# Kernel tuning notes

Measured on AMD Instinct MI355X. Metric: run time of the kernel, lower is better.

## Reference

```python
import jax, jax.numpy as jnp
import numpy as np

MS0 = 4            # base sector size (ms[0])
MS1 = 4            # top sector size (r=[1] -> ms[-1]=ms0)
Q = 2              # q_length (Ising spin states)
C = 512            # c_length
LAYERS = 2
B = 256
L = 16
FS = MS0 * MS0 - 1  # neighborhood size, excludes target pixel


def setup_inputs():
    key = jax.random.key(0)
    ks = jax.random.split(key, 8)
    v = jax.random.randint(ks[0], (B, L, L), 0, Q, dtype=jnp.int32)
    u = v.astype(jnp.float32)
    emb = jax.random.normal(ks[1], (FS, Q, C), dtype=jnp.float32)  # fs embedding tables

    def lin_w(k, out_d, in_d):
        b = 1.0 / np.sqrt(in_d)
        return jax.random.uniform(k, (out_d, in_d), minval=-b, maxval=b, dtype=jnp.float32)

    def lin_b(k, out_d, in_d):
        b = 1.0 / np.sqrt(in_d)
        return jax.random.uniform(k, (out_d,), minval=-b, maxval=b, dtype=jnp.float32)

    k2a, k2b = jax.random.split(ks[2])
    k3a, k3b = jax.random.split(ks[3])
    mlp_w1 = lin_w(k2a, C, C)
    mlp_b1 = lin_b(k2b, C, C)
    mlp_w2 = lin_w(k3a, Q, C)
    mlp_b2 = lin_b(k3b, Q, C)

    def lstm_p(k, in_d):
        k1, k2, k3, k4 = jax.random.split(k, 4)
        b = 1.0 / np.sqrt(C)
        wi = jax.random.uniform(k1, (4 * C, in_d), minval=-b, maxval=b, dtype=jnp.float32)
        wh = jax.random.uniform(k2, (4 * C, C), minval=-b, maxval=b, dtype=jnp.float32)
        bi = jax.random.uniform(k3, (4 * C,), minval=-b, maxval=b, dtype=jnp.float32)
        bh = jax.random.uniform(k4, (4 * C,), minval=-b, maxval=b, dtype=jnp.float32)
        return wi, wh, bi, bh

    w_ih0, w_hh0, b_ih0, b_hh0 = lstm_p(ks[4], MS1 * MS1)
    w_ih1, w_hh1, b_ih1, b_hh1 = lstm_p(ks[5], C)
    return dict(u=u, v=v, emb=emb,
                mlp_w1=mlp_w1, mlp_b1=mlp_b1, mlp_w2=mlp_w2, mlp_b2=mlp_b2,
                w_ih0=w_ih0, w_hh0=w_hh0, b_ih0=b_ih0, b_hh0=b_hh0,
                w_ih1=w_ih1, w_hh1=w_hh1, b_ih1=b_ih1, b_hh1=b_hh1)


def _forward(u, v, emb, mlp_w1, mlp_b1, mlp_w2, mlp_b2,
             w_ih0, w_hh0, b_ih0, b_hh0, w_ih1, w_hh1, b_ih1, b_hh1):
    n_sec = L // MS0
    margin = MS0 - 1
    lstm_params = ((w_ih0, w_hh0, b_ih0, b_hh0), (w_ih1, w_hh1, b_ih1, b_hh1))

    def lstm_step(x, state):
        # single-timestep multi-layer LSTM (eval mode, no dropout)
        h, c = state  # [LAYERS, B, C] each
        hs, cs = [], []
        inp = x
        for l, (wi, wh, bi, bh) in enumerate(lstm_params):
            g = inp @ wi.T + bi + h[l] @ wh.T + bh
            gi, gf, gg, go = jnp.split(g, 4, axis=-1)  # torch gate order i,f,g,o
            cn = jax.nn.sigmoid(gf) * c[l] + jax.nn.sigmoid(gi) * jnp.tanh(gg)
            hn = jax.nn.sigmoid(go) * jnp.tanh(cn)
            hs.append(hn)
            cs.append(cn)
            inp = hn
        return (jnp.stack(hs), jnp.stack(cs))

    zeros_state = lambda: (jnp.zeros((LAYERS, B, C), jnp.float32),
                           jnp.zeros((LAYERS, B, C), jnp.float32))
    memi = [zeros_state() for _ in range(n_sec)]
    memj = [zeros_state() for _ in range(n_sec)]
    sector = [0, 0]
    softout = jnp.zeros((B, L, L, Q), jnp.float32)
    nbr = jnp.arange(FS)[None, :]  # [1, FS] embedding-table indices
    key = jax.random.key(1234)

    for i in range(n_sec - 1):
        for j in range(n_sec - 1):
            si, sj = i * MS0, j * MS0
            ns0, ns1 = MS1 * (si // MS1), MS1 * (sj // MS1)
            if ns1 != sector[1]:
                sector = [ns0, ns1]
                for s in range(n_sec):
                    uv = u[:, s * MS1:(s + 1) * MS1, sector[1]:sector[1] + MS1].reshape(B, MS1 * MS1)
                    memj[s] = lstm_step(uv, memj[s])
            if ns0 != sector[0]:
                sector[0] = ns0
                uv = u[:, sector[0] - MS1:sector[0], sector[1]:sector[1] + MS1].reshape(B, MS1 * MS1)
                memi[sector[0] // MS1] = lstm_step(uv, memi[sector[0] // MS1])
            h0 = memj[i][0][0] + memi[j][0][0]  # layer-0 hidden sum, [B, C]
            for ii in range(MS0):
                for jj in range(MS0):
                    a, b = si + ii + 1, sj + jj + 1
                    pr, pc = a + margin, b + margin  # target pixel (bottom-right of patch)
                    patch = v[:, a:a + MS0, b:b + MS0].reshape(B, MS0 * MS0)[:, :FS]  # mask drops (margin,margin)
                    xemb = emb[nbr, patch, :].sum(axis=1)  # [B, C]
                    z = jax.nn.relu((xemb + h0) @ mlp_w1.T + mlp_b1)
                    logits = jax.nn.log_softmax(z @ mlp_w2.T + mlp_b2, axis=-1)  # [B, Q]
                    softout = softout.at[:, pr, pc].set(logits)
                    key, sub = jax.random.split(key)
                    samp = jax.random.categorical(sub, logits, axis=-1)  # [B]
                    v = v.at[:, pr, pc].set(samp.astype(v.dtype))
                    u = u.at[:, pr, pc].set(samp.astype(u.dtype))
    return softout, u, v


def reference(u, v, emb, mlp_w1, mlp_b1, mlp_w2, mlp_b2,
              w_ih0, w_hh0, b_ih0, b_hh0, w_ih1, w_hh1, b_ih1, b_hh1):
    return _forward(u, v, emb, mlp_w1, mlp_b1, mlp_w2, mlp_b2,
                    w_ih0, w_hh0, b_ih0, b_hh0, w_ih1, w_hh1, b_ih1, b_hh1)
```

## Files before the change

kernel.cpp:

```cpp
#include <hip/hip_runtime.h>
#include <cstdint>
#include <cstddef>

constexpr int NB = 256;
constexpr int NC = 512;
constexpr int NL = 16;
constexpr int NFS = 15;

#define PARTITIONABLE 1

struct TFOut { uint32_t a, b; };

__host__ __device__ constexpr uint32_t rotl32(uint32_t x, int d) {
  return (x << d) | (x >> (32 - d));
}

__host__ __device__ constexpr TFOut tf2x32(uint32_t k0, uint32_t k1,
                                           uint32_t x0, uint32_t x1) {
  uint32_t k2 = k0 ^ k1 ^ 0x1BD11BDAu;
  x0 += k0; x1 += k1;
  const int R0[4] = {13, 15, 26, 6};
  const int R1[4] = {17, 29, 16, 24};
  for (int i = 0; i < 4; i++) { x0 += x1; x1 = rotl32(x1, R0[i]); x1 ^= x0; }
  x0 += k1; x1 += k2 + 1u;
  for (int i = 0; i < 4; i++) { x0 += x1; x1 = rotl32(x1, R1[i]); x1 ^= x0; }
  x0 += k2; x1 += k0 + 2u;
  for (int i = 0; i < 4; i++) { x0 += x1; x1 = rotl32(x1, R0[i]); x1 ^= x0; }
  x0 += k0; x1 += k1 + 3u;
  for (int i = 0; i < 4; i++) { x0 += x1; x1 = rotl32(x1, R1[i]); x1 ^= x0; }
  x0 += k1; x1 += k2 + 4u;
  for (int i = 0; i < 4; i++) { x0 += x1; x1 = rotl32(x1, R0[i]); x1 ^= x0; }
  x0 += k2; x1 += k0 + 5u;
  return TFOut{x0, x1};
}

struct SubKeys { uint32_t v[288]; };

constexpr SubKeys make_subkeys() {
  SubKeys s{};
  uint32_t k0 = 0u, k1 = 1234u;
  for (int t = 0; t < 144; t++) {
#if PARTITIONABLE
    TFOut nk = tf2x32(k0, k1, 0u, 0u);
    TFOut sk = tf2x32(k0, k1, 0u, 1u);
    s.v[2 * t] = sk.a; s.v[2 * t + 1] = sk.b;
    k0 = nk.a; k1 = nk.b;
#else
    TFOut p0 = tf2x32(k0, k1, 0u, 2u);
    TFOut p1 = tf2x32(k0, k1, 1u, 3u);
    s.v[2 * t] = p0.b; s.v[2 * t + 1] = p1.b;
    k0 = p0.a; k1 = p1.a;
#endif
  }
  return s;
}

__constant__ SubKeys SUBKEYS = make_subkeys();

__device__ __forceinline__ float gumbel_from_bits(uint32_t bits) {
  uint32_t ub = (bits >> 9) | 0x3f800000u;
  float f = __uint_as_float(ub) - 1.0f;
  float u = (f == 0.0f) ? 1.17549435e-38f : f;
  float inner = logf(u);
  float outer = logf(-inner);
  return -outer;
}

typedef __attribute__((ext_vector_type(8))) short bf16x8;
typedef __attribute__((ext_vector_type(4))) float f32x4;

__device__ __forceinline__ void gl2lds16(const unsigned short* g,
                                         unsigned short* l) {
  __builtin_amdgcn_global_load_lds(
      (const __attribute__((address_space(1))) unsigned int*)g,
      (__attribute__((address_space(3))) unsigned int*)l, 16, 0, 0);
}

__device__ __forceinline__ uint32_t bf_rne(float x) {
  uint32_t u = __float_as_uint(x);
  return (u + 0x7fffu + ((u >> 16) & 1u)) >> 16;
}

__device__ __forceinline__ uint32_t bfpack2(float a, float b) {
  return (bf_rne(a) & 0xffffu) | (bf_rne(b) << 16);
}

__global__ __launch_bounds__(256) void setup_kernel(
    const float* __restrict__ u_in, const int* __restrict__ v_in,
    float* __restrict__ h0buf, float* __restrict__ cbuf,
    float* __restrict__ u_cur, int* __restrict__ v_cur,
    float* __restrict__ out_soft, float* __restrict__ out_u,
    float* __restrict__ out_v, unsigned int* __restrict__ az) {
  int idx = blockIdx.x * 256 + threadIdx.x;
  h0buf[idx] = 0.0f;
  if (idx < 3 * NB * NC) cbuf[idx] = 0.0f;
  if (idx < 393216) az[idx] = 0u;
  if (idx < NB * NL * NL) {
    float uv = u_in[idx];
    int vv = v_in[idx];
    u_cur[idx] = uv;
    v_cur[idx] = vv;
    out_u[idx] = uv;
    out_v[idx] = (float)vv;
  }
  if (idx < NB * NL * NL * 2) out_soft[idx] = 0.0f;
}

__global__ __launch_bounds__(256) void split_w_kernel(
    const float* __restrict__ whh, const float* __restrict__ wih,
    unsigned short* __restrict__ Bhi, unsigned short* __restrict__ Blo,
    unsigned short* __restrict__ Buh, unsigned short* __restrict__ Bul) {
  int idx = blockIdx.x * 256 + threadIdx.x;
  float x = whh[idx];
  uint32_t hb = bf_rne(x);
  float lo = x - __uint_as_float(hb << 16);
  Bhi[idx] = (unsigned short)hb;
  Blo[idx] = (unsigned short)bf_rne(lo);
  if (idx < 2048 * 16) {
    float y = wih[idx];
    uint32_t hb2 = bf_rne(y);
    float lo2 = y - __uint_as_float(hb2 << 16);
    Buh[idx] = (unsigned short)hb2;
    Bul[idx] = (unsigned short)bf_rne(lo2);
  }
}

__global__ __launch_bounds__(256) void wd_kernel(
    const float* __restrict__ emb, const float* __restrict__ w1,
    const float* __restrict__ b1, float* __restrict__ WD,
    float* __restrict__ A0v) {
  __shared__ double dvec[NC];
  int n = blockIdx.x, tid = threadIdx.x;
  for (int k = tid; k < NC; k += 256) {
    if (n < NFS) {
      dvec[k] = (double)emb[(n * 2 + 1) * NC + k] - (double)emb[(n * 2) * NC + k];
    } else {
      double s = 0.0;
      for (int nn = 0; nn < NFS; nn++) s += (double)emb[(nn * 2) * NC + k];
      dvec[k] = s;
    }
  }
  __syncthreads();
  for (int c = tid; c < NC; c += 256) {
    double acc = 0.0;
    const float* wrow = w1 + (size_t)c * NC;
    for (int k = 0; k < NC; k++) acc += dvec[k] * (double)wrow[k];
    if (n < NFS) WD[n * NC + c] = (float)acc;
    else         A0v[c] = (float)(acc + (double)b1[c]);
  }
}

__global__ __launch_bounds__(256) void lstm_mfma_kernel(
    const unsigned short* __restrict__ Ahi, const unsigned short* __restrict__ Alo,
    const unsigned short* __restrict__ Bhi, const unsigned short* __restrict__ Blo,
    const unsigned short* __restrict__ Buh, const unsigned short* __restrict__ Bul,
    const float* __restrict__ u_cur, float* __restrict__ gpart, int col0) {
  __shared__ __align__(16) unsigned short Ah[128 * 32];
  __shared__ __align__(16) unsigned short Al[128 * 32];
  __shared__ __align__(16) unsigned short Bh[64 * 32];
  __shared__ __align__(16) unsigned short Bl[64 * 32];

  int bx = blockIdx.x;
  int kz = bx & 3;
  int ct = (bx >> 2) & 31;
  int rt = bx >> 7;
  int tid = threadIdx.x;
  int w = tid >> 6, lane = tid & 63;
  int wm = w >> 1, wn = w & 1;
  int row0 = rt * 128;
  int n0 = ct * 64;
  int l15 = lane & 15, kg = lane >> 4;

  f32x4 acc[4][2];
#pragma unroll
  for (int i = 0; i < 4; i++)
#pragma unroll
    for (int j = 0; j < 2; j++) acc[i][j] = (f32x4){0.f, 0.f, 0.f, 0.f};

  bool first = true;

  if (kz == 0) {
    int r = tid >> 1, half = tid & 1;
    int s = rt >> 1;
    int b = (rt & 1) * 128 + r;
    const float* up = u_cur + b * 256 + (s * 4 + half * 2) * 16 + col0;
    float4 f0 = *(const float4*)up;
    float4 f1 = *(const float4*)(up + 16);
    int4 dat;
    dat.x = (int)bfpack2(f0.x, f0.y);
    dat.y = (int)bfpack2(f0.z, f0.w);
    dat.z = (int)bfpack2(f1.x, f1.y);
    dat.w = (int)bfpack2(f1.z, f1.w);
    *(int4*)&Ah[r * 32 + half * 8] = dat;
    *(int4*)&Ah[r * 32 + 16 + half * 8] = (int4){0, 0, 0, 0};
    int t2 = tid & 127;
    int br = t2 >> 1, bh = t2 & 1;
    const unsigned short* bsrc =
        (tid < 128 ? Buh : Bul) + (size_t)(n0 + br) * 16 + bh * 8;
    unsigned short* bdst = (tid < 128 ? Bh : Bl);
    *(int4*)&bdst[br * 32 + bh * 8] = *(const int4*)bsrc;
    *(int4*)&bdst[br * 32 + 16 + bh * 8] = (int4){0, 0, 0, 0};
    __syncthreads();
    bf16x8 a[4], bb[2];
#pragma unroll
    for (int i = 0; i < 4; i++)
      a[i] = *(const bf16x8*)&Ah[(wm * 64 + i * 16 + l15) * 32 + kg * 8];
#pragma unroll
    for (int j = 0; j < 2; j++)
      bb[j] = *(const bf16x8*)&Bh[(wn * 32 + j * 16 + l15) * 32 + kg * 8];
#pragma unroll
    for (int i = 0; i < 4; i++)
#pragma unroll
      for (int j = 0; j < 2; j++)
        acc[i][j] = __builtin_amdgcn_mfma_f32_16x16x32_bf16(a[i], bb[j],
                                                            acc[i][j], 0, 0, 0);
#pragma unroll
    for (int j = 0; j < 2; j++)
      bb[j] = *(const bf16x8*)&Bl[(wn * 32 + j * 16 + l15) * 32 + kg * 8];
#pragma unroll
    for (int i = 0; i < 4; i++)
#pragma unroll
      for (int j = 0; j < 2; j++)
        acc[i][j] = __builtin_amdgcn_mfma_f32_16x16x32_bf16(a[i], bb[j],
                                                            acc[i][j], 0, 0, 0);
    first = false;
  }

  for (int kc = 0; kc < 4; kc++) {
    int k0 = kz * 128 + kc * 32;
    if (!first) __syncthreads();
    first = false;
#pragma unroll
    for (int q = 0; q < 2; q++) {
      int slot = (w * 2 + q) * 64 + lane;
      int r = slot >> 2, c2 = slot & 3;
      size_t so = (size_t)(row0 + r) * 512 + k0 + c2 * 8;
      gl2lds16(Ahi + so, &Ah[(size_t)(w * 2 + q) * 512]);
      gl2lds16(Alo + so, &Al[(size_t)(w * 2 + q) * 512]);
    }
    {
      int slot = w * 64 + lane;
      int r = slot >> 2, c2 = slot & 3;
      size_t so = (size_t)(n0 + r) * 512 + k0 + c2 * 8;
      gl2lds16(Bhi + so, &Bh[(size_t)w * 512]);
      gl2lds16(Blo + so, &Bl[(size_t)w * 512]);
    }
    __syncthreads();
    bf16x8 ah[4], al[4], bh2[2], bl2[2];
#pragma unroll
    for (int i = 0; i < 4; i++) {
      int ro = (wm * 64 + i * 16 + l15) * 32 + kg * 8;
      ah[i] = *(const bf16x8*)&Ah[ro];
      al[i] = *(const bf16x8*)&Al[ro];
    }
#pragma unroll
    for (int j = 0; j < 2; j++) {
      int ro = (wn * 32 + j * 16 + l15) * 32 + kg * 8;
      bh2[j] = *(const bf16x8*)&Bh[ro];
      bl2[j] = *(const bf16x8*)&Bl[ro];
    }
#pragma unroll
    for (int i = 0; i < 4; i++)
#pragma unroll
      for (int j = 0; j < 2; j++) {
        acc[i][j] = __builtin_amdgcn_mfma_f32_16x16x32_bf16(ah[i], bh2[j],
                                                            acc[i][j], 0, 0, 0);
        acc[i][j] = __builtin_amdgcn_mfma_f32_16x16x32_bf16(ah[i], bl2[j],
                                                            acc[i][j], 0, 0, 0);
        acc[i][j] = __builtin_amdgcn_mfma_f32_16x16x32_bf16(al[i], bh2[j],
                                                            acc[i][j], 0, 0, 0);
      }
  }

  float* gp = gpart + (size_t)kz * 768 * 2048;
  int rbase = row0 + wm * 64;
  int cbase = n0 + wn * 32;
#pragma unroll
  for (int i = 0; i < 4; i++)
#pragma unroll
    for (int j = 0; j < 2; j++)
#pragma unroll
      for (int rr = 0; rr < 4; rr++) {
        int grow = rbase + i * 16 + kg * 4 + rr;
        int gcol = cbase + j * 16 + l15;
        gp[(size_t)grow * 2048 + gcol] = acc[i][j][rr];
      }
}

__global__ __launch_bounds__(256) void lstm_gates_kernel(
    const float* __restrict__ gpart, const float* __restrict__ bih,
    const float* __restrict__ bhh, float* __restrict__ h_out,
    float* __restrict__ cbuf, unsigned short* __restrict__ Ahi,
    unsigned short* __restrict__ Alo) {
  int idx = blockIdx.x * 256 + threadIdx.x;
  int row = idx >> 9, c = idx & 511;
  const size_t P = (size_t)768 * 2048;
  size_t base = (size_t)row * 2048 + c;
  float gv[4];
#pragma unroll
  for (int g = 0; g < 4; g++) {
    int nidx = g * 512 + c;
    float v = bih[nidx] + bhh[nidx];
#pragma unroll
    for (int kzz = 0; kzz < 4; kzz++)
      v += gpart[(size_t)kzz * P + base + g * 512];
    gv[g] = v;
  }
  size_t off = (size_t)row * NC + c;
  float c_old = cbuf[off];
  float sig_i = 1.0f / (1.0f + expf(-gv[0]));
  float sig_f = 1.0f / (1.0f + expf(-gv[1]));
  float tg    = tanhf(gv[2]);
  float sig_o = 1.0f / (1.0f + expf(-gv[3]));
  float cn = sig_f * c_old + sig_i * tg;
  float hn = sig_o * tanhf(cn);
  cbuf[off] = cn;
  h_out[off] = hn;
  uint32_t hb = bf_rne(hn);
  float lo = hn - __uint_as_float(hb << 16);
  Ahi[off] = (unsigned short)hb;
  Alo[off] = (unsigned short)bf_rne(lo);
}

__global__ __launch_bounds__(256) void w1h0_kernel(
    const float* __restrict__ h_in,
    const float* __restrict__ w1, float* __restrict__ Hpart) {
  int bx = blockIdx.x;
  int ks = bx >> 5;
  int bt = (bx >> 3) & 3;
  int ct = bx & 7;
  int tid = threadIdx.x, tn = tid & 15, tb = tid >> 4;

  __shared__ float hs[64][36];
  __shared__ float wt[64][36];
  float acc[4][4] = {};
  const float* hbase = h_in + (size_t)(bt * 64) * NC;

  for (int kc = 0; kc < 2; kc++) {
    int k0 = ks * 64 + kc * 32;
    __syncthreads();
    for (int t = 0; t < 2; t++) {
      int idx = tid + t * 256;
      int row = idx >> 3, kk4 = idx & 7;
      *(float4*)&hs[row][kk4 * 4] =
          *(const float4*)(hbase + (size_t)row * NC + k0 + kk4 * 4);
      int wrow = ct * 64 + row;
      *(float4*)&wt[row][kk4 * 4] =
          *(const float4*)(w1 + (size_t)wrow * NC + k0 + kk4 * 4);
    }
    __syncthreads();
#pragma unroll
    for (int kk4 = 0; kk4 < 8; kk4++) {
      float4 hv[4], wv[4];
#pragma unroll
      for (int i = 0; i < 4; i++) hv[i] = *(float4*)&hs[tb * 4 + i][kk4 * 4];
#pragma unroll
      for (int j = 0; j < 4; j++) wv[j] = *(float4*)&wt[tn + 16 * j][kk4 * 4];
#pragma unroll
      for (int i = 0; i < 4; i++)
#pragma unroll
        for (int j = 0; j < 4; j++)
          acc[i][j] += hv[i].x * wv[j].x + hv[i].y * wv[j].y +
                       hv[i].z * wv[j].z + hv[i].w * wv[j].w;
    }
  }
#pragma unroll
  for (int i = 0; i < 4; i++) {
    int b = bt * 64 + tb * 4 + i;
#pragma unroll
    for (int j = 0; j < 4; j++) {
      int cidx = ct * 64 + tn + 16 * j;
      Hpart[((size_t)ks * NB + b) * NC + cidx] = acc[i][j];
    }
  }
}

__global__ __launch_bounds__(64) void pixel_kernel(
    const float* __restrict__ WD, const float* __restrict__ A0v,
    const float* __restrict__ Hpart, const float* __restrict__ w2,
    const float* __restrict__ b2, float* __restrict__ u_cur,
    int* __restrict__ v_cur, float* __restrict__ out_soft,
    float* __restrict__ out_u, float* __restrict__ out_v,
    int si, int sj, int t_base) {
  int b = blockIdx.x, lane = threadIdx.x;
  __shared__ float gum[32];

  int widx = (lane < 49) ? lane : 48;
  int vv = v_cur[b * 256 + (si + 1 + widx / 7) * 16 + (sj + 1 + widx % 7)];
  unsigned long long mask = __ballot((lane < 49) && (vv != 0));

  if (lane < 32) {
    int t = t_base + (lane >> 1);
    uint32_t sk0 = SUBKEYS.v[2 * t], sk1 = SUBKEYS.v[2 * t + 1];
    uint32_t bits;
#if PARTITIONABLE
    TFOut o = tf2x32(sk0, sk1, 0u, (uint32_t)(2 * b + (lane & 1)));
    bits = o.a ^ o.b;
#else
    uint32_t f = (uint32_t)(2 * b + (lane & 1));
    if (f < 256u) { TFOut o = tf2x32(sk0, sk1, f, f + 256u); bits = o.a; }
    else          { TFOut o = tf2x32(sk0, sk1, f - 256u, f); bits = o.b; }
#endif
    gum[lane] = gumbel_from_bits(bits);
  }

  float wdreg[NFS][8];
#pragma unroll
  for (int n = 0; n < NFS; n++)
#pragma unroll
    for (int r = 0; r < 8; r++) wdreg[n][r] = WD[n * NC + lane + 64 * r];

  float w2r0[8], w2r1[8];
#pragma unroll
  for (int r = 0; r < 8; r++) {
    w2r0[r] = w2[lane + 64 * r];
    w2r1[r] = w2[NC + lane + 64 * r];
  }
  double b20 = (double)b2[0], b21 = (double)b2[1];

  float base[8];
#pragma unroll
  for (int r = 0; r < 8; r++) {
    int c = lane + 64 * r;
    float v = A0v[c];
#pragma unroll
    for (int ks = 0; ks < 8; ks++) v += Hpart[((size_t)ks * NB + b) * NC + c];
    base[r] = v;
  }
  __syncthreads();

#pragma unroll 1
  for (int ii = 0; ii < 4; ii++) {
#pragma unroll 1
    for (int jj = 0; jj < 4; jj++) {
      int bofs = ii * 7 + jj;
      float acc[8];
#pragma unroll
      for (int r = 0; r < 8; r++) acc[r] = base[r];
#pragma unroll
      for (int n = 0; n < NFS; n++) {
        const int OFF = (n / 4) * 7 + (n % 4);
        float pf = (float)((unsigned)((mask >> (bofs + OFF)) & 1ull));
#pragma unroll
        for (int r = 0; r < 8; r++) acc[r] = fmaf(pf, wdreg[n][r], acc[r]);
      }
      double d0 = 0.0, d1 = 0.0;
#pragma unroll
      for (int r = 0; r < 8; r++) {
        float z = fmaxf(acc[r], 0.0f);
        d0 += (double)z * (double)w2r0[r];
        d1 += (double)z * (double)w2r1[r];
      }
#pragma unroll
      for (int off = 32; off > 0; off >>= 1) {
        d0 += __shfl_xor(d0, off, 64);
        d1 += __shfl_xor(d1, off, 64);
      }
      float r0 = (float)(d0 + b20);
      float r1 = (float)(d1 + b21);
      float m = fmaxf(r0, r1);
      float s0 = r0 - m, s1 = r1 - m;
      float lse = logf(expf(s0) + expf(s1));
      float l0 = s0 - lse, l1 = s1 - lse;
      int pidx = ii * 4 + jj;
      float a0 = l0 + gum[2 * pidx];
      float a1 = l1 + gum[2 * pidx + 1];
      int samp = (a1 > a0) ? 1 : 0;
      int tbit = bofs + 24;
      mask = (mask & ~(1ull << tbit)) | ((unsigned long long)samp << tbit);
      if (lane == 0) {
        int pr = si + ii + 4, pc = sj + jj + 4;
        size_t so = ((size_t)(b * 16 + pr) * 16 + pc) * 2;
        out_soft[so] = l0;
        out_soft[so + 1] = l1;
        int po = b * 256 + pr * 16 + pc;
        float fs = (float)samp;
        u_cur[po] = fs;
        v_cur[po] = samp;
        out_u[po] = fs;
        out_v[po] = fs;
      }
    }
  }
}

extern "C" void kernel_launch(void* const* d_in, const int* in_sizes, int n_in,
                              void* d_out, int out_size, void* d_ws,
                              size_t ws_size, hipStream_t stream) {
  (void)in_sizes; (void)n_in; (void)out_size; (void)ws_size;
  const float* u_in = (const float*)d_in[0];
  const int*   v_in = (const int*)d_in[1];
  const float* emb  = (const float*)d_in[2];
  const float* w1   = (const float*)d_in[3];
  const float* b1   = (const float*)d_in[4];
  const float* w2   = (const float*)d_in[5];
  const float* b2   = (const float*)d_in[6];
  const float* wih  = (const float*)d_in[7];
  const float* whh  = (const float*)d_in[8];
  const float* bih  = (const float*)d_in[9];
  const float* bhh  = (const float*)d_in[10];

  float* ws = (float*)d_ws;
  const size_t HP = (size_t)4 * NB * NC;
  float* h0buf = ws;
  float* cbuf  = h0buf + 2 * HP;
  float* gpart = cbuf + (size_t)3 * NB * NC;
  float* Hpart = gpart + (size_t)4 * 768 * 2048;
  float* WDp   = Hpart + (size_t)8 * NB * NC;
  float* A0v   = WDp + NFS * NC;
  float* u_cur = A0v + NC;
  int*   v_cur = (int*)(u_cur + NB * NL * NL);
  unsigned short* Ahi = (unsigned short*)(v_cur + NB * NL * NL);
  unsigned short* Alo = Ahi + (size_t)768 * 512;
  unsigned short* Bhi = Alo + (size_t)768 * 512;
  unsigned short* Blo = Bhi + (size_t)2048 * 512;
  unsigned short* Buh = Blo + (size_t)2048 * 512;
  unsigned short* Bul = Buh + (size_t)2048 * 16;

  float* out_soft = (float*)d_out;
  float* out_u = out_soft + NB * NL * NL * 2;
  float* out_v = out_u + NB * NL * NL;

  setup_kernel<<<dim3(4096), dim3(256), 0, stream>>>(
      u_in, v_in, h0buf, cbuf, u_cur, v_cur, out_soft, out_u, out_v,
      (unsigned int*)Ahi);
  split_w_kernel<<<dim3(4096), dim3(256), 0, stream>>>(
      whh, wih, Bhi, Blo, Buh, Bul);
  wd_kernel<<<dim3(16), dim3(256), 0, stream>>>(emb, w1, b1, WDp, A0v);

  for (int k = 0; k < 9; k++) {
    if (k > 0) {
      int e = k - 1;
      int col0 = (e % 3 == 0) ? 4 : ((e % 3 == 1) ? 8 : 0);
      lstm_mfma_kernel<<<dim3(768), dim3(256), 0, stream>>>(
          Ahi, Alo, Bhi, Blo, Buh, Bul, u_cur, gpart, col0);
      lstm_gates_kernel<<<dim3(1536), dim3(256), 0, stream>>>(
          gpart, bih, bhh, h0buf + (size_t)((e & 1) ^ 1) * HP, cbuf, Ahi, Alo);
    }
    w1h0_kernel<<<dim3(256), dim3(256), 0, stream>>>(
        h0buf + (size_t)(k & 1) * HP + (size_t)(k / 3) * NB * NC, w1, Hpart);
    pixel_kernel<<<dim3(256), dim3(64), 0, stream>>>(
        WDp, A0v, Hpart, w2, b2, u_cur, v_cur, out_soft, out_u, out_v,
        (k / 3) * 4, (k % 3) * 4, k * 16);
  }
}
```

Baseline: 486.2 us.

## Fuse LSTM GEMM with gate epilogue using full-K tiles and double buffering

Replaces the split-K MFMA kernel plus separate gates kernel with one kernel. Each single-wave block computes all four gates for a 64-row by 16-column tile over the full K range, then applies the LSTM cell update in registers. The A operands are ping-ponged between two buffers, because other blocks still read the previous h while this one writes the new one. LDS staging is double-buffered with an XOR swizzle. This removes the gpart round trip and one launch per step, at the cost of only 384 single-wave blocks and a longer serial K loop per block.

```diff
diff --git a/kernel.cpp b/kernel.cpp
--- a/kernel.cpp
+++ b/kernel.cpp
@@ -92,9 +92,9 @@
     float* __restrict__ out_soft, float* __restrict__ out_u,
     float* __restrict__ out_v, unsigned int* __restrict__ az) {
   int idx = blockIdx.x * 256 + threadIdx.x;
-  h0buf[idx] = 0.0f;
+  if (idx < 786432) h0buf[idx] = 0.0f;
   if (idx < 3 * NB * NC) cbuf[idx] = 0.0f;
-  if (idx < 393216) az[idx] = 0u;
+  if (idx < 786432) az[idx] = 0u;
   if (idx < NB * NL * NL) {
     float uv = u_in[idx];
     int vv = v_in[idx];
@@ -150,176 +150,176 @@
   }
 }
 
-__global__ __launch_bounds__(256) void lstm_mfma_kernel(
-    const unsigned short* __restrict__ Ahi, const unsigned short* __restrict__ Alo,
+__device__ __forceinline__ void stage_chunk(
+    const unsigned short* __restrict__ Ah_r,
+    const unsigned short* __restrict__ Al_r,
+    const unsigned short* __restrict__ Bh_r,
+    const unsigned short* __restrict__ Bl_r,
+    unsigned short* sA, unsigned short* sAl,
+    unsigned short* sB, unsigned short* sBl,
+    int lane, int row0, int ct, int k0) {
+#pragma unroll
+  for (int cc = 0; cc < 4; cc++) {
+    int row = cc * 16 + (lane >> 2);
+    int c2 = (lane & 3) ^ ((row >> 1) & 3);
+    size_t aso = (size_t)(row0 + row) * 512 + k0 + c2 * 8;
+    gl2lds16(Ah_r + aso, &sA[cc * 512]);
+    gl2lds16(Al_r + aso, &sAl[cc * 512]);
+    int n = (row >> 4) * 512 + ct * 16 + (row & 15);
+    size_t bso = (size_t)n * 512 + k0 + c2 * 8;
+    gl2lds16(Bh_r + bso, &sB[cc * 512]);
+    gl2lds16(Bl_r + bso, &sBl[cc * 512]);
+  }
+}
+
+__global__ __launch_bounds__(64) void lstm_fused_kernel(
+    const unsigned short* __restrict__ Ah_r, const unsigned short* __restrict__ Al_r,
+    unsigned short* __restrict__ Ah_w, unsigned short* __restrict__ Al_w,
     const unsigned short* __restrict__ Bhi, const unsigned short* __restrict__ Blo,
     const unsigned short* __restrict__ Buh, const unsigned short* __restrict__ Bul,
-    const float* __restrict__ u_cur, float* __restrict__ gpart, int col0) {
-  __shared__ __align__(16) unsigned short Ah[128 * 32];
-  __shared__ __align__(16) unsigned short Al[128 * 32];
-  __shared__ __align__(16) unsigned short Bh[64 * 32];
-  __shared__ __align__(16) unsigned short Bl[64 * 32];
+    const float* __restrict__ u_cur, const float* __restrict__ bih,
+    const float* __restrict__ bhh, float* __restrict__ cbuf,
+    float* __restrict__ h_out, int col0) {
+  __shared__ __align__(16) unsigned short sA[2][64 * 32];
+  __shared__ __align__(16) unsigned short sAl[2][64 * 32];
+  __shared__ __align__(16) unsigned short sB[2][64 * 32];
+  __shared__ __align__(16) unsigned short sBl[2][64 * 32];
 
   int bx = blockIdx.x;
-  int kz = bx & 3;
-  int ct = (bx >> 2) & 31;
-  int rt = bx >> 7;
-  int tid = threadIdx.x;
-  int w = tid >> 6, lane = tid & 63;
-  int wm = w >> 1, wn = w & 1;
-  int row0 = rt * 128;
-  int n0 = ct * 64;
+  int rt = bx >> 5;
+  int ct = bx & 31;
+  int lane = threadIdx.x;
   int l15 = lane & 15, kg = lane >> 4;
-
-  f32x4 acc[4][2];
+  int row0 = rt * 64;
+  int sct = rt >> 2;
+  int sw = (l15 >> 1) & 3;
+
+  f32x4 acc[4][4];
 #pragma unroll
   for (int i = 0; i < 4; i++)
 #pragma unroll
-    for (int j = 0; j < 2; j++) acc[i][j] = (f32x4){0.f, 0.f, 0.f, 0.f};
-
-  bool first = true;
-
-  if (kz == 0) {
-    int r = tid >> 1, half = tid & 1;
-    int s = rt >> 1;
-    int b = (rt & 1) * 128 + r;
-    const float* up = u_cur + b * 256 + (s * 4 + half * 2) * 16 + col0;
-    float4 f0 = *(const float4*)up;
+    for (int g = 0; g < 4; g++) acc[i][g] = (f32x4){0.f, 0.f, 0.f, 0.f};
+
+  {
+    int r = lane;
+    int rsw = (r >> 1) & 3;
+    int b = (rt & 3) * 64 + r;
+    const float* up = u_cur + b * 256 + sct * 64 + col0;
+    float4 f0 = *(const float4*)(up);
     float4 f1 = *(const float4*)(up + 16);
-    int4 dat;
-    dat.x = (int)bfpack2(f0.x, f0.y);
-    dat.y = (int)bfpack2(f0.z, f0.w);
-    dat.z = (int)bfpack2(f1.x, f1.y);
-    dat.w = (int)bfpack2(f1.z, f1.w);
-    *(int4*)&Ah[r * 32 + half * 8] = dat;
-    *(int4*)&Ah[r * 32 + 16 + half * 8] = (int4){0, 0, 0, 0};
-    int t2 = tid & 127;
-    int br = t2 >> 1, bh = t2 & 1;
-    const unsigned short* bsrc =
-        (tid < 128 ? Buh : Bul) + (size_t)(n0 + br) * 16 + bh * 8;
-    unsigned short* bdst = (tid < 128 ? Bh : Bl);
-    *(int4*)&bdst[br * 32 + bh * 8] = *(const int4*)bsrc;
-    *(int4*)&bdst[br * 32 + 16 + bh * 8] = (int4){0, 0, 0, 0};
+    float4 f2 = *(const float4*)(up + 32);
+    float4 f3 = *(const float4*)(up + 48);
+    int4 d0, d1;
+    d0.x = (int)bfpack2(f0.x, f0.y); d0.y = (int)bfpack2(f0.z, f0.w);
+    d0.z = (int)bfpack2(f1.x, f1.y); d0.w = (int)bfpack2(f1.z, f1.w);
+    d1.x = (int)bfpack2(f2.x, f2.y); d1.y = (int)bfpack2(f2.z, f2.w);
+    d1.z = (int)bfpack2(f3.x, f3.y); d1.w = (int)bfpack2(f3.z, f3.w);
+    int4 z4 = {0, 0, 0, 0};
+    *(int4*)&sA[0][r * 32 + (0 ^ rsw) * 8] = d0;
+    *(int4*)&sA[0][r * 32 + (1 ^ rsw) * 8] = d1;
+    *(int4*)&sA[0][r * 32 + (2 ^ rsw) * 8] = z4;
+    *(int4*)&sA[0][r * 32 + (3 ^ rsw) * 8] = z4;
+    int n = (r >> 4) * 512 + ct * 16 + (r & 15);
+    int4 u0 = *(const int4*)&Buh[n * 16];
+    int4 u1 = *(const int4*)&Buh[n * 16 + 8];
+    *(int4*)&sB[0][r * 32 + (0 ^ rsw) * 8] = u0;
+    *(int4*)&sB[0][r * 32 + (1 ^ rsw) * 8] = u1;
+    *(int4*)&sB[0][r * 32 + (2 ^ rsw) * 8] = z4;
+    *(int4*)&sB[0][r * 32 + (3 ^ rsw) * 8] = z4;
+    int4 w0 = *(const int4*)&Bul[n * 16];
+    int4 w1v = *(const int4*)&Bul[n * 16 + 8];
+    *(int4*)&sBl[0][r * 32 + (0 ^ rsw) * 8] = w0;
+    *(int4*)&sBl[0][r * 32 + (1 ^ rsw) * 8] = w1v;
+    *(int4*)&sBl[0][r * 32 + (2 ^ rsw) * 8] = z4;
+    *(int4*)&sBl[0][r * 32 + (3 ^ rsw) * 8] = z4;
+  }
+  __syncthreads();
+  stage_chunk(Ah_r, Al_r, Bhi, Blo, sA[1], sAl[1], sB[1], sBl[1],
+              lane, row0, ct, 0);
+  {
+    bf16x8 a[4], bh[4], bl[4];
+#pragma unroll
+    for (int i = 0; i < 4; i++)
+      a[i] = *(const bf16x8*)&sA[0][(i * 16 + l15) * 32 + (kg ^ sw) * 8];
+#pragma unroll
+    for (int g = 0; g < 4; g++) {
+      bh[g] = *(const bf16x8*)&sB[0][(g * 16 + l15) * 32 + (kg ^ sw) * 8];
+      bl[g] = *(const bf16x8*)&sBl[0][(g * 16 + l15) * 32 + (kg ^ sw) * 8];
+    }
+#pragma unroll
+    for (int i = 0; i < 4; i++)
+#pragma unroll
+      for (int g = 0; g < 4; g++) {
+        acc[i][g] = __builtin_amdgcn_mfma_f32_16x16x32_bf16(a[i], bh[g],
+                                                            acc[i][g], 0, 0, 0);
+        acc[i][g] = __builtin_amdgcn_mfma_f32_16x16x32_bf16(a[i], bl[g],
+                                                            acc[i][g], 0, 0, 0);
+      }
+  }
+
+  for (int t = 0; t < 16; t++) {
     __syncthreads();
-    bf16x8 a[4], bb[2];
+    if (t < 15)
+      stage_chunk(Ah_r, Al_r, Bhi, Blo, sA[t & 1], sAl[t & 1], sB[t & 1],
+                  sBl[t & 1], lane, row0, ct, (t + 1) * 32);
+    int cur = (t ^ 1) & 1;
+    bf16x8 ah[4], al[4], bh[4], bl[4];
+#pragma unroll
+    for (int i = 0; i < 4; i++) {
+      int ro = (i * 16 + l15) * 32 + (kg ^ sw) * 8;
+      ah[i] = *(const bf16x8*)&sA[cur][ro];
+      al[i] = *(const bf16x8*)&sAl[cur][ro];
+    }
+#pragma unroll
+    for (int g = 0; g < 4; g++) {
+      int ro = (g * 16 + l15) * 32 + (kg ^ sw) * 8;
+      bh[g] = *(const bf16x8*)&sB[cur][ro];
+      bl[g] = *(const bf16x8*)&sBl[cur][ro];
+    }
 #pragma unroll
     for (int i = 0; i < 4; i++)
-      a[i] = *(const bf16x8*)&Ah[(wm * 64 + i * 16 + l15) * 32 + kg * 8];
-#pragma unroll
-    for (int j = 0; j < 2; j++)
-      bb[j] = *(const bf16x8*)&Bh[(wn * 32 + j * 16 + l15) * 32 + kg * 8];
-#pragma unroll
-    for (int i = 0; i < 4; i++)
-#pragma unroll
-      for (int j = 0; j < 2; j++)
-        acc[i][j] = __builtin_amdgcn_mfma_f32_16x16x32_bf16(a[i], bb[j],
-                                                            acc[i][j], 0, 0, 0);
-#pragma unroll
-    for (int j = 0; j < 2; j++)
-      bb[j] = *(const bf16x8*)&Bl[(wn * 32 + j * 16 + l15) * 32 + kg * 8];
-#pragma unroll
-    for (int i = 0; i < 4; i++)
-#pragma unroll
-      for (int j = 0; j < 2; j++)
-        acc[i][j] = __builtin_amdgcn_mfma_f32_16x16x32_bf16(a[i], bb[j],
-                                                            acc[i][j], 0, 0, 0);
-    first = false;
-  }
-
-  for (int kc = 0; kc < 4; kc++) {
-    int k0 = kz * 128 + kc * 32;
-    if (!first) __syncthreads();
-    first = false;
-#pragma unroll
-    for (int q = 0; q < 2; q++) {
-      int slot = (w * 2 + q) * 64 + lane;
-      int r = slot >> 2, c2 = slot & 3;
-      size_t so = (size_t)(row0 + r) * 512 + k0 + c2 * 8;
-      gl2lds16(Ahi + so, &Ah[(size_t)(w * 2 + q) * 512]);
-      gl2lds16(Alo + so, &Al[(size_t)(w * 2 + q) * 512]);
-    }
-    {
-      int slot = w * 64 + lane;
-      int r = slot >> 2, c2 = slot & 3;
-      size_t so = (size_t)(n0 + r) * 512 + k0 + c2 * 8;
-      gl2lds16(Bhi + so, &Bh[(size_t)w * 512]);
-      gl2lds16(Blo + so, &Bl[(size_t)w * 512]);
-    }
-    __syncthreads();
-    bf16x8 ah[4], al[4], bh2[2], bl2[2];
-#pragma unroll
-    for (int i = 0; i < 4; i++) {
-      int ro = (wm * 64 + i * 16 + l15) * 32 + kg * 8;
-      ah[i] = *(const bf16x8*)&Ah[ro];
-      al[i] = *(const bf16x8*)&Al[ro];
-    }
-#pragma unroll
-    for (int j = 0; j < 2; j++) {
-      int ro = (wn * 32 + j * 16 + l15) * 32 + kg * 8;
-      bh2[j] = *(const bf16x8*)&Bh[ro];
-      bl2[j] = *(const bf16x8*)&Bl[ro];
-    }
-#pragma unroll
-    for (int i = 0; i < 4; i++)
-#pragma unroll
-      for (int j = 0; j < 2; j++) {
-        acc[i][j] = __builtin_amdgcn_mfma_f32_16x16x32_bf16(ah[i], bh2[j],
-                                                            acc[i][j], 0, 0, 0);
-        acc[i][j] = __builtin_amdgcn_mfma_f32_16x16x32_bf16(ah[i], bl2[j],
-                                                            acc[i][j], 0, 0, 0);
-        acc[i][j] = __builtin_amdgcn_mfma_f32_16x16x32_bf16(al[i], bh2[j],
-                                                            acc[i][j], 0, 0, 0);
+#pragma unroll
+      for (int g = 0; g < 4; g++) {
+        acc[i][g] = __builtin_amdgcn_mfma_f32_16x16x32_bf16(ah[i], bh[g],
+                                                            acc[i][g], 0, 0, 0);
+        acc[i][g] = __builtin_amdgcn_mfma_f32_16x16x32_bf16(ah[i], bl[g],
+                                                            acc[i][g], 0, 0, 0);
+        acc[i][g] = __builtin_amdgcn_mfma_f32_16x16x32_bf16(al[i], bh[g],
+                                                            acc[i][g], 0, 0, 0);
       }
   }
 
-  float* gp = gpart + (size_t)kz * 768 * 2048;
-  int rbase = row0 + wm * 64;
-  int cbase = n0 + wn * 32;
+  int c = ct * 16 + l15;
+  float bi_[4], bh_[4];
+#pragma unroll
+  for (int g = 0; g < 4; g++) {
+    bi_[g] = bih[g * 512 + c];
+    bh_[g] = bhh[g * 512 + c];
+  }
 #pragma unroll
   for (int i = 0; i < 4; i++)
 #pragma unroll
-    for (int j = 0; j < 2; j++)
-#pragma unroll
-      for (int rr = 0; rr < 4; rr++) {
-        int grow = rbase + i * 16 + kg * 4 + rr;
-        int gcol = cbase + j * 16 + l15;
-        gp[(size_t)grow * 2048 + gcol] = acc[i][j][rr];
-      }
-}
-
-__global__ __launch_bounds__(256) void lstm_gates_kernel(
-    const float* __restrict__ gpart, const float* __restrict__ bih,
-    const float* __restrict__ bhh, float* __restrict__ h_out,
-    float* __restrict__ cbuf, unsigned short* __restrict__ Ahi,
-    unsigned short* __restrict__ Alo) {
-  int idx = blockIdx.x * 256 + threadIdx.x;
-  int row = idx >> 9, c = idx & 511;
-  const size_t P = (size_t)768 * 2048;
-  size_t base = (size_t)row * 2048 + c;
-  float gv[4];
-#pragma unroll
-  for (int g = 0; g < 4; g++) {
-    int nidx = g * 512 + c;
-    float v = bih[nidx] + bhh[nidx];
-#pragma unroll
-    for (int kzz = 0; kzz < 4; kzz++)
-      v += gpart[(size_t)kzz * P + base + g * 512];
-    gv[g] = v;
-  }
-  size_t off = (size_t)row * NC + c;
-  float c_old = cbuf[off];
-  float sig_i = 1.0f / (1.0f + expf(-gv[0]));
-  float sig_f = 1.0f / (1.0f + expf(-gv[1]));
-  float tg    = tanhf(gv[2]);
-  float sig_o = 1.0f / (1.0f + expf(-gv[3]));
-  float cn = sig_f * c_old + sig_i * tg;
-  float hn = sig_o * tanhf(cn);
-  cbuf[off] = cn;
-  h_out[off] = hn;
-  uint32_t hb = bf_rne(hn);
-  float lo = hn - __uint_as_float(hb << 16);
-  Ahi[off] = (unsigned short)hb;
-  Alo[off] = (unsigned short)bf_rne(lo);
+    for (int rr = 0; rr < 4; rr++) {
+      int row = row0 + i * 16 + kg * 4 + rr;
+      size_t off = (size_t)row * 512 + c;
+      float c_old = cbuf[off];
+      float g0 = acc[i][0][rr] + bi_[0] + bh_[0];
+      float g1 = acc[i][1][rr] + bi_[1] + bh_[1];
+      float g2 = acc[i][2][rr] + bi_[2] + bh_[2];
+      float g3 = acc[i][3][rr] + bi_[3] + bh_[3];
+      float sig_i = 1.0f / (1.0f + expf(-g0));
+      float sig_f = 1.0f / (1.0f + expf(-g1));
+      float tg    = tanhf(g2);
+      float sig_o = 1.0f / (1.0f + expf(-g3));
+      float cn = sig_f * c_old + sig_i * tg;
+      float hn = sig_o * tanhf(cn);
+      cbuf[off] = cn;
+      h_out[off] = hn;
+      uint32_t hb = bf_rne(hn);
+      float lo = hn - __uint_as_float(hb << 16);
+      Ah_w[off] = (unsigned short)hb;
+      Al_w[off] = (unsigned short)bf_rne(lo);
+    }
 }
 
 __global__ __launch_bounds__(256) void w1h0_kernel(
@@ -501,21 +501,21 @@
   const float* bhh  = (const float*)d_in[10];
 
   float* ws = (float*)d_ws;
-  const size_t HP = (size_t)4 * NB * NC;
+  const size_t HP = (size_t)3 * NB * NC;
   float* h0buf = ws;
   float* cbuf  = h0buf + 2 * HP;
-  float* gpart = cbuf + (size_t)3 * NB * NC;
-  float* Hpart = gpart + (size_t)4 * 768 * 2048;
+  float* Hpart = cbuf + (size_t)3 * NB * NC;
   float* WDp   = Hpart + (size_t)8 * NB * NC;
   float* A0v   = WDp + NFS * NC;
   float* u_cur = A0v + NC;
   int*   v_cur = (int*)(u_cur + NB * NL * NL);
   unsigned short* Ahi = (unsigned short*)(v_cur + NB * NL * NL);
-  unsigned short* Alo = Ahi + (size_t)768 * 512;
-  unsigned short* Bhi = Alo + (size_t)768 * 512;
+  unsigned short* Alo = Ahi + (size_t)2 * 768 * 512;
+  unsigned short* Bhi = Alo + (size_t)2 * 768 * 512;
   unsigned short* Blo = Bhi + (size_t)2048 * 512;
   unsigned short* Buh = Blo + (size_t)2048 * 512;
   unsigned short* Bul = Buh + (size_t)2048 * 16;
+  const size_t APAR = (size_t)768 * 512;
 
   float* out_soft = (float*)d_out;
   float* out_u = out_soft + NB * NL * NL * 2;
@@ -532,10 +532,12 @@
     if (k > 0) {
       int e = k - 1;
       int col0 = (e % 3 == 0) ? 4 : ((e % 3 == 1) ? 8 : 0);
-      lstm_mfma_kernel<<<dim3(768), dim3(256), 0, stream>>>(
-          Ahi, Alo, Bhi, Blo, Buh, Bul, u_cur, gpart, col0);
-      lstm_gates_kernel<<<dim3(1536), dim3(256), 0, stream>>>(
-          gpart, bih, bhh, h0buf + (size_t)((e & 1) ^ 1) * HP, cbuf, Ahi, Alo);
+      int rp = e & 1, wp = rp ^ 1;
+      lstm_fused_kernel<<<dim3(384), dim3(64), 0, stream>>>(
+          Ahi + (size_t)rp * APAR, Alo + (size_t)rp * APAR,
+          Ahi + (size_t)wp * APAR, Alo + (size_t)wp * APAR,
+          Bhi, Blo, Buh, Bul, u_cur, bih, bhh, cbuf,
+          h0buf + (size_t)wp * HP, col0);
     }
     w1h0_kernel<<<dim3(256), dim3(256), 0, stream>>>(
         h0buf + (size_t)(k & 1) * HP + (size_t)(k / 3) * NB * NC, w1, Hpart);
```

After: 547.0 us. +12.5%, slower.
